# Kernel optimization log

Hardware: AMD Instinct MI355X
Metric: run time of the kernel (lower is better)

## Reference

```python
import jax, jax.numpy as jnp
import numpy as np

N_NODES = 100000


def gcn_conv(x, src, dst, W, b, n_nodes):
    """PyG GCNConv: out = D^{-1/2} (A + I) D^{-1/2} X W + b (self-loops added)."""
    h = x @ W  # [N, out]
    loops = jnp.arange(n_nodes, dtype=src.dtype)
    s = jnp.concatenate([src, loops])
    d = jnp.concatenate([dst, loops])
    deg = jax.ops.segment_sum(jnp.ones_like(d, dtype=h.dtype), d, num_segments=n_nodes)
    dinv = jnp.where(deg > 0, jax.lax.rsqrt(deg), 0.0)
    norm = dinv[s] * dinv[d]  # [E+N]
    msgs = norm[:, None] * h[s]  # gather + scale
    out = jax.ops.segment_sum(msgs, d, num_segments=n_nodes)
    return out + b


def setup_inputs() -> dict:
    key = jax.random.key(0)
    ks = jax.random.split(key, 10)
    n, e, f_in = N_NODES, 1600000, 128
    x = jax.random.normal(ks[0], (n, f_in), dtype=jnp.float32)
    edge_index = jax.random.randint(ks[1], (2, e), 0, n, dtype=jnp.int64)
    dims = [f_in, 15, 20, 27, 36]
    params = {}
    for i in range(4):
        fan_in, fan_out = dims[i], dims[i + 1]
        scale = 1.0 / np.sqrt(fan_in)
        params[f"W{i+1}"] = jax.random.uniform(ks[2 + 2 * i], (fan_in, fan_out), minval=-scale, maxval=scale, dtype=jnp.float32)
        params[f"b{i+1}"] = jax.random.uniform(ks[3 + 2 * i], (fan_out,), minval=-scale, maxval=scale, dtype=jnp.float32)
    return {"x": x, "edge_index": edge_index, **params}


def reference(x, edge_index, W1, b1, W2, b2, W3, b3, W4, b4):
    src, dst = edge_index[0], edge_index[1]
    n = x.shape[0]
    h = jax.nn.selu(gcn_conv(x, src, dst, W1, b1, n))
    h = jax.nn.selu(gcn_conv(h, src, dst, W2, b2, n))
    h = jax.nn.selu(gcn_conv(h, src, dst, W3, b3, n))
    h = jax.nn.selu(gcn_conv(h, src, dst, W4, b4, n))
    return h
```

## Files before the change

kernel.cpp:

```cpp
#include <hip/hip_runtime.h>
#include <hip/hip_fp16.h>
#include <math.h>

#define BLK 256
#define CBSH 9
#define CBN 512
#define NCBC 256
#define NB2 512

__device__ __forceinline__ float selu_f(float x) {
    const float kScale = 1.0507009873554805f;
    const float kAlpha = 1.6732632423543772f;
    return x > 0.0f ? kScale * x : kScale * kAlpha * expm1f(x);
}

__device__ __forceinline__ float2 h2f2(unsigned u) {
    __half2 h = *reinterpret_cast<__half2*>(&u);
    return __half22float2(h);
}
__device__ __forceinline__ void h8_set(float* a, uint4 v) {
    float2 f0 = h2f2(v.x), f1 = h2f2(v.y), f2 = h2f2(v.z), f3 = h2f2(v.w);
    a[0] = f0.x; a[1] = f0.y; a[2] = f1.x; a[3] = f1.y;
    a[4] = f2.x; a[5] = f2.y; a[6] = f3.x; a[7] = f3.y;
}
__device__ __forceinline__ void h8_add(float* a, uint4 v) {
    float2 f0 = h2f2(v.x), f1 = h2f2(v.y), f2 = h2f2(v.z), f3 = h2f2(v.w);
    a[0] += f0.x; a[1] += f0.y; a[2] += f1.x; a[3] += f1.y;
    a[4] += f2.x; a[5] += f2.y; a[6] += f3.x; a[7] += f3.y;
}

__global__ void k_cnt(const int* __restrict__ dst, int* __restrict__ H, int e, int nbkt) {
    __shared__ int hist[NCBC];
    int tid = threadIdx.x;
    for (int b = tid; b < nbkt; b += BLK) hist[b] = 0;
    __syncthreads();
    int per = (e + NB2 - 1) / NB2;
    int lo = blockIdx.x * per;
    int hi = min(e, lo + per);
    for (int i = lo + tid; i < hi; i += BLK) atomicAdd(&hist[dst[i] >> CBSH], 1);
    __syncthreads();
    for (int b = tid; b < nbkt; b += BLK) H[blockIdx.x * nbkt + b] = hist[b];
}

__global__ void k_bsum(const int* __restrict__ H, int* __restrict__ bstart, int nbkt, int e) {
    __shared__ int tot[NCBC];
    int tid = threadIdx.x;
    for (int b = tid; b < nbkt; b += BLK) {
        int s = 0;
        for (int i = 0; i < NB2; ++i) s += H[i * nbkt + b];
        tot[b] = s;
    }
    __syncthreads();
    if (tid == 0) {
        int acc = 0;
        for (int b = 0; b < nbkt; ++b) {
            bstart[b] = acc;
            acc += tot[b];
        }
        bstart[nbkt] = acc;
    }
}

__global__ void k_off(int* __restrict__ H, const int* __restrict__ bstart, int nbkt) {
    __shared__ int lds[BLK];
    int b = blockIdx.x, tid = threadIdx.x;
    int v0 = H[(2 * tid) * nbkt + b];
    int v1 = H[(2 * tid + 1) * nbkt + b];
    int pair = v0 + v1;
    lds[tid] = pair;
    __syncthreads();
    int val = pair;
    for (int off = 1; off < BLK; off <<= 1) {
        int t2 = (tid >= off) ? lds[tid - off] : 0;
        __syncthreads();
        val += t2;
        lds[tid] = val;
        __syncthreads();
    }
    int excl = val - pair + bstart[b];
    H[(2 * tid) * nbkt + b] = excl;
    H[(2 * tid + 1) * nbkt + b] = excl + v0;
}

__global__ void k_scatter2(const int* __restrict__ src, const int* __restrict__ dst,
                           const int* __restrict__ H, unsigned* __restrict__ slab,
                           int e, int nbkt) {
    __shared__ int cur[NCBC];
    int tid = threadIdx.x;
    for (int b = tid; b < nbkt; b += BLK) cur[b] = H[blockIdx.x * nbkt + b];
    __syncthreads();
    int per = (e + NB2 - 1) / NB2;
    int lo = blockIdx.x * per;
    int hi = min(e, lo + per);
    for (int i = lo + tid; i < hi; i += BLK) {
        int s = src[i], d = dst[i];
        int b = d >> CBSH;
        int pos = atomicAdd(&cur[b], 1);
        slab[pos] = ((unsigned)s << CBSH) | (unsigned)(d & (CBN - 1));
    }
}

__global__ void k_build(const int* __restrict__ bstart, const unsigned* __restrict__ slab,
                        int* __restrict__ rowptr, float* __restrict__ dinv,
                        int* __restrict__ csr, int n, int e) {
    __shared__ int hist[CBN];
    __shared__ int stmp[BLK];
    int b = blockIdx.x, tid = threadIdx.x;
    hist[2 * tid] = 0;
    hist[2 * tid + 1] = 0;
    __syncthreads();
    int lo = bstart[b], hi = bstart[b + 1];
    for (int i = lo + tid; i < hi; i += BLK) atomicAdd(&hist[slab[i] & (CBN - 1)], 1);
    __syncthreads();
    int h0 = hist[2 * tid], h1 = hist[2 * tid + 1];
    int pair = h0 + h1;
    stmp[tid] = pair;
    __syncthreads();
    int val = pair;
    for (int off = 1; off < BLK; off <<= 1) {
        int t2 = (tid >= off) ? stmp[tid - off] : 0;
        __syncthreads();
        val += t2;
        stmp[tid] = val;
        __syncthreads();
    }
    int e0 = lo + val - pair;
    int e1 = e0 + h0;
    hist[2 * tid] = e0;
    hist[2 * tid + 1] = e1;
    int node0 = b << CBSH;
    int nA = node0 + 2 * tid, nB = nA + 1;
    if (nA < n) { rowptr[nA] = e0; dinv[nA] = rsqrtf((float)(h0 + 1)); }
    if (nB < n) { rowptr[nB] = e1; dinv[nB] = rsqrtf((float)(h1 + 1)); }
    if (b == 0 && tid == 0) rowptr[n] = e;
    __syncthreads();
    for (int i = lo + tid; i < hi; i += BLK) {
        unsigned p = slab[i];
        int pos = atomicAdd(&hist[p & (CBN - 1)], 1);
        csr[pos] = (int)(p >> CBSH);
    }
}

template <int K, int KP, int F, int SI, int SO, bool FUSE_IN>
__global__ void k_gemm(const float* __restrict__ xin, const float* __restrict__ W,
                       const float* __restrict__ bprev, const float* __restrict__ dinv,
                       __half* __restrict__ hs, int n) {
    constexpr int F8 = (F + 7) & ~7;
    int i = blockIdx.x * BLK + threadIdx.x;
    if (i >= n) return;
    const float* xr = xin + (size_t)i * SI;
    float di = dinv[i];
    float accf[F8];
#pragma unroll
    for (int f = 0; f < F8; ++f) accf[f] = 0.0f;
#pragma unroll
    for (int k4 = 0; k4 < KP / 4; ++k4) {
        float4 xv = *reinterpret_cast<const float4*>(xr + k4 * 4);
        float xs4[4] = {xv.x, xv.y, xv.z, xv.w};
#pragma unroll
        for (int j = 0; j < 4; ++j) {
            const int k = k4 * 4 + j;
            if (k < K) {
                float xval = xs4[j];
                if (FUSE_IN) xval = selu_f(di * xval + bprev[k]);
#pragma unroll
                for (int f = 0; f < F; ++f) accf[f] = fmaf(xval, W[k * F + f], accf[f]);
            }
        }
    }
#pragma unroll
    for (int f = 0; f < F; ++f) accf[f] *= di;
    __half2* ro2 = reinterpret_cast<__half2*>(hs + (size_t)i * SO);
#pragma unroll
    for (int f2 = 0; f2 < F8 / 2; ++f2)
        ro2[f2] = __float22half2_rn(make_float2(accf[2 * f2], accf[2 * f2 + 1]));
}

__global__ void k_gemm4(const float* __restrict__ xin, const float* __restrict__ W,
                        const float* __restrict__ bprev, const float* __restrict__ dinv,
                        __half* __restrict__ hsm, __half* __restrict__ hst, int n) {
    constexpr int K = 27, F = 36;
    int i = blockIdx.x * BLK + threadIdx.x;
    if (i >= n) return;
    const float* xr = xin + (size_t)i * 32;
    float di = dinv[i];
    float accf[40];
#pragma unroll
    for (int f = 0; f < 40; ++f) accf[f] = 0.0f;
#pragma unroll
    for (int k4 = 0; k4 < 7; ++k4) {
        float4 xv = *reinterpret_cast<const float4*>(xr + k4 * 4);
        float xs4[4] = {xv.x, xv.y, xv.z, xv.w};
#pragma unroll
        for (int j = 0; j < 4; ++j) {
            const int k = k4 * 4 + j;
            if (k < K) {
                float xval = selu_f(di * xv.x + bprev[k]);
                xval = selu_f(di * xs4[j] + bprev[k]);
#pragma unroll
                for (int f = 0; f < F; ++f) accf[f] = fmaf(xval, W[k * F + f], accf[f]);
            }
        }
    }
#pragma unroll
    for (int f = 0; f < F; ++f) accf[f] *= di;
    __half2* rm = reinterpret_cast<__half2*>(hsm + (size_t)i * 32);
#pragma unroll
    for (int f2 = 0; f2 < 16; ++f2)
        rm[f2] = __float22half2_rn(make_float2(accf[2 * f2], accf[2 * f2 + 1]));
    __half2* rt = reinterpret_cast<__half2*>(hst + (size_t)i * 8);
#pragma unroll
    for (int f2 = 0; f2 < 4; ++f2)
        rt[f2] = __float22half2_rn(make_float2(accf[32 + 2 * f2], accf[32 + 2 * f2 + 1]));
}

template <int F, int S , int G, int SOUT>
__global__ void k_agg(const int* __restrict__ rowptr, const int* __restrict__ csr,
                      const __half* __restrict__ hs, float* __restrict__ out, int n) {
    constexpr int NPW = 64 / G;
    constexpr int CH = ((F + 7) & ~7) / 8;
    int lane = threadIdx.x & 63;
    int g = lane / G;
    int fl = lane & (G - 1);
    int wid = (blockIdx.x * BLK + threadIdx.x) >> 6;
    int d = wid * NPW + g;
    if (d >= n || fl >= CH) return;
    int beg = rowptr[d], end = rowptr[d + 1];
    auto rowp = [&](int r) {
        return reinterpret_cast<const uint4*>(hs + (size_t)r * S) + fl;
    };
    float s0[8], s1[8] = {0}, s2[8] = {0}, s3[8] = {0};
    h8_set(s0, *rowp(d));
    int p = beg;
    for (; p + 8 <= end; p += 8) {
        int e0 = __builtin_nontemporal_load(csr + p);
        int e1 = __builtin_nontemporal_load(csr + p + 1);
        int e2 = __builtin_nontemporal_load(csr + p + 2);
        int e3 = __builtin_nontemporal_load(csr + p + 3);
        int e4 = __builtin_nontemporal_load(csr + p + 4);
        int e5 = __builtin_nontemporal_load(csr + p + 5);
        int e6 = __builtin_nontemporal_load(csr + p + 6);
        int e7 = __builtin_nontemporal_load(csr + p + 7);
        uint4 v0 = *rowp(e0), v1 = *rowp(e1), v2 = *rowp(e2), v3 = *rowp(e3);
        uint4 v4 = *rowp(e4), v5 = *rowp(e5), v6 = *rowp(e6), v7 = *rowp(e7);
        h8_add(s0, v0); h8_add(s1, v1); h8_add(s2, v2); h8_add(s3, v3);
        h8_add(s0, v4); h8_add(s1, v5); h8_add(s2, v6); h8_add(s3, v7);
    }
    for (; p + 4 <= end; p += 4) {
        int e0 = __builtin_nontemporal_load(csr + p);
        int e1 = __builtin_nontemporal_load(csr + p + 1);
        int e2 = __builtin_nontemporal_load(csr + p + 2);
        int e3 = __builtin_nontemporal_load(csr + p + 3);
        uint4 v0 = *rowp(e0), v1 = *rowp(e1), v2 = *rowp(e2), v3 = *rowp(e3);
        h8_add(s0, v0); h8_add(s1, v1); h8_add(s2, v2); h8_add(s3, v3);
    }
    for (; p < end; ++p) h8_add(s0, *rowp(__builtin_nontemporal_load(csr + p)));
    float sum[8];
#pragma unroll
    for (int j = 0; j < 8; ++j) sum[j] = (s0[j] + s1[j]) + (s2[j] + s3[j]);
    float* op = out + (size_t)d * SOUT + fl * 8;
    *reinterpret_cast<float4*>(op) = make_float4(sum[0], sum[1], sum[2], sum[3]);
    *reinterpret_cast<float4*>(op + 4) = make_float4(sum[4], sum[5], sum[6], sum[7]);
}

__global__ void k_agg4(const int* __restrict__ rowptr, const int* __restrict__ csr,
                       const __half* __restrict__ hsm, const __half* __restrict__ hst,
                       float* __restrict__ out, const float* __restrict__ dinv,
                       const float* __restrict__ bias, int n) {
    constexpr int G = 8, NPW = 8;
    int lane = threadIdx.x & 63;
    int g = lane / G;
    int fl = lane & (G - 1);
    int wid = (blockIdx.x * BLK + threadIdx.x) >> 6;
    int d = wid * NPW + g;
    if (d >= n || fl >= 5) return;
    int beg = rowptr[d], end = rowptr[d + 1];
    const __half* bp = (fl < 4) ? hsm + fl * 8 : hst;
    int mul = (fl < 4) ? 32 : 8;
    auto rowp = [&](int r) {
        return reinterpret_cast<const uint4*>(bp + (size_t)r * mul);
    };
    float s0[8], s1[8] = {0}, s2[8] = {0}, s3[8] = {0};
    h8_set(s0, *rowp(d));
    int p = beg;
    for (; p + 8 <= end; p += 8) {
        int e0 = __builtin_nontemporal_load(csr + p);
        int e1 = __builtin_nontemporal_load(csr + p + 1);
        int e2 = __builtin_nontemporal_load(csr + p + 2);
        int e3 = __builtin_nontemporal_load(csr + p + 3);
        int e4 = __builtin_nontemporal_load(csr + p + 4);
        int e5 = __builtin_nontemporal_load(csr + p + 5);
        int e6 = __builtin_nontemporal_load(csr + p + 6);
        int e7 = __builtin_nontemporal_load(csr + p + 7);
        uint4 v0 = *rowp(e0), v1 = *rowp(e1), v2 = *rowp(e2), v3 = *rowp(e3);
        uint4 v4 = *rowp(e4), v5 = *rowp(e5), v6 = *rowp(e6), v7 = *rowp(e7);
        h8_add(s0, v0); h8_add(s1, v1); h8_add(s2, v2); h8_add(s3, v3);
        h8_add(s0, v4); h8_add(s1, v5); h8_add(s2, v6); h8_add(s3, v7);
    }
    for (; p + 4 <= end; p += 4) {
        int e0 = __builtin_nontemporal_load(csr + p);
        int e1 = __builtin_nontemporal_load(csr + p + 1);
        int e2 = __builtin_nontemporal_load(csr + p + 2);
        int e3 = __builtin_nontemporal_load(csr + p + 3);
        uint4 v0 = *rowp(e0), v1 = *rowp(e1), v2 = *rowp(e2), v3 = *rowp(e3);
        h8_add(s0, v0); h8_add(s1, v1); h8_add(s2, v2); h8_add(s3, v3);
    }
    for (; p < end; ++p) h8_add(s0, *rowp(__builtin_nontemporal_load(csr + p)));
    float dv = dinv[d];
    float r[8];
#pragma unroll
    for (int j = 0; j < 8; ++j) {
        float sum = (s0[j] + s1[j]) + (s2[j] + s3[j]);
        int col = (fl < 4) ? fl * 8 + j : 32 + j;
        r[j] = (col < 36) ? selu_f(dv * sum + bias[col]) : 0.0f;
    }
    if (fl < 4) {
        float* op = out + (size_t)d * 36 + fl * 8;
        *reinterpret_cast<float4*>(op) = make_float4(r[0], r[1], r[2], r[3]);
        *reinterpret_cast<float4*>(op + 4) = make_float4(r[4], r[5], r[6], r[7]);
    } else {
        float* op = out + (size_t)d * 36 + 32;
        *reinterpret_cast<float4*>(op) = make_float4(r[0], r[1], r[2], r[3]);
    }
}

extern "C" void kernel_launch(void* const* d_in, const int* in_sizes, int n_in,
                              void* d_out, int out_size, void* d_ws, size_t ws_size,
                              hipStream_t stream) {
    const float* x = (const float*)d_in[0];
    const int* ei = (const int*)d_in[1];
    const float* W1 = (const float*)d_in[2];
    const float* b1 = (const float*)d_in[3];
    const float* W2 = (const float*)d_in[4];
    const float* b2 = (const float*)d_in[5];
    const float* W3 = (const float*)d_in[6];
    const float* b3 = (const float*)d_in[7];
    const float* W4 = (const float*)d_in[8];
    const float* b4 = (const float*)d_in[9];

    int n = in_sizes[0] / 128;
    int e = in_sizes[1] / 2;
    const int* s32 = ei;
    const int* d32 = ei + e;
    int nbkt = (n + CBN - 1) >> CBSH;

    char* w = (char*)d_ws;
    auto alloc = [&](size_t bytes) {
        char* p = w;
        w += (bytes + 255) & ~(size_t)255;
        return p;
    };
    int* rowptr = (int*)alloc(((size_t)n + 1) * 4);
    float* dinv = (float*)alloc((size_t)n * 4);
    int* csr = (int*)alloc((size_t)e * 4);
    int* H = (int*)alloc((size_t)NB2 * nbkt * 4);
    int* bstart = (int*)alloc(((size_t)nbkt + 1) * 4);
    __half* bufA = (__half*)alloc((size_t)n * 40 * 2);
    float* bufB = (float*)alloc((size_t)n * 32 * 4);
    unsigned* slab = (unsigned*)bufA;
    __half* hsm = bufA;
    __half* hst = bufA + (size_t)n * 32;

    int nb = (n + BLK - 1) / BLK;

    k_cnt<<<NB2, BLK, 0, stream>>>(d32, H, e, nbkt);
    k_bsum<<<1, BLK, 0, stream>>>(H, bstart, nbkt, e);
    k_off<<<nbkt, BLK, 0, stream>>>(H, bstart, nbkt);
    k_scatter2<<<NB2, BLK, 0, stream>>>(s32, d32, H, slab, e, nbkt);
    k_build<<<nbkt, BLK, 0, stream>>>(bstart, slab, rowptr, dinv, csr, n, e);

    int ab1 = (n + 127) / 128;
    int ab2 = (n + 63) / 64;
    int ab4 = (n + 31) / 32;

    k_gemm<128, 128, 15, 128, 16, false><<<nb, BLK, 0, stream>>>(x, W1, nullptr, dinv, bufA, n);
    k_agg<15, 16, 2, 16><<<ab1, BLK, 0, stream>>>(rowptr, csr, bufA, bufB, n);

    k_gemm<15, 16, 20, 16, 32, true><<<nb, BLK, 0, stream>>>(bufB, W2, b1, dinv, bufA, n);
    k_agg<20, 32, 4, 32><<<ab2, BLK, 0, stream>>>(rowptr, csr, bufA, bufB, n);

    k_gemm<20, 20, 27, 32, 32, true><<<nb, BLK, 0, stream>>>(bufB, W3, b2, dinv, bufA, n);
    k_agg<27, 32, 4, 32><<<ab2, BLK, 0, stream>>>(rowptr, csr, bufA, bufB, n);

    k_gemm4<<<nb, BLK, 0, stream>>>(bufB, W4, b3, dinv, hsm, hst, n);
    k_agg4<<<ab4, BLK, 0, stream>>>(rowptr, csr, hsm, hst, (float*)d_out, dinv, b4, n);
}
```

Before: 277.4 us.

## Reorder GCN layers to aggregate before transform using chunked fp16 feature layout

Layers 2-4 now aggregate the smaller input features first and apply the weight matrix afterwards (A·X then W), since for growing widths (15→20→27→36) aggregating narrower inputs moves fewer bytes per edge. Features are stored in a chunk-major layout of 8-half uint4 slices, with one thread per node per chunk, in place of the wavefront-group gather. The normalisation, bias and SELU are fused into the transform epilogue. The cost is an extra fp32 intermediate buffer and more blocks that each re-read the CSR indices once per chunk.

```diff
diff --git a/kernel.cpp b/kernel.cpp
--- a/kernel.cpp
+++ b/kernel.cpp
@@ -27,6 +27,18 @@
     float2 f0 = h2f2(v.x), f1 = h2f2(v.y), f2 = h2f2(v.z), f3 = h2f2(v.w);
     a[0] += f0.x; a[1] += f0.y; a[2] += f1.x; a[3] += f1.y;
     a[4] += f2.x; a[5] += f2.y; a[6] += f3.x; a[7] += f3.y;
+}
+__device__ __forceinline__ uint4 f8_pack(const float* a) {
+    __half2 h0 = __float22half2_rn(make_float2(a[0], a[1]));
+    __half2 h1 = __float22half2_rn(make_float2(a[2], a[3]));
+    __half2 h2 = __float22half2_rn(make_float2(a[4], a[5]));
+    __half2 h3 = __float22half2_rn(make_float2(a[6], a[7]));
+    uint4 u;
+    u.x = *reinterpret_cast<unsigned*>(&h0);
+    u.y = *reinterpret_cast<unsigned*>(&h1);
+    u.z = *reinterpret_cast<unsigned*>(&h2);
+    u.w = *reinterpret_cast<unsigned*>(&h3);
+    return u;
 }
 
 __global__ void k_cnt(const int* __restrict__ dst, int* __restrict__ H, int e, int nbkt) {
@@ -141,187 +153,145 @@
     }
 }
 
-template <int K, int KP, int F, int SI, int SO, bool FUSE_IN>
-__global__ void k_gemm(const float* __restrict__ xin, const float* __restrict__ W,
-                       const float* __restrict__ bprev, const float* __restrict__ dinv,
-                       __half* __restrict__ hs, int n) {
-    constexpr int F8 = (F + 7) & ~7;
+
+__global__ void k_gemm1(const float* __restrict__ x, const float* __restrict__ W,
+                        const float* __restrict__ dinv, uint4* __restrict__ G, int n) {
     int i = blockIdx.x * BLK + threadIdx.x;
     if (i >= n) return;
-    const float* xr = xin + (size_t)i * SI;
+    const float* xr = x + (size_t)i * 128;
+    float acc[16];
+#pragma unroll
+    for (int f = 0; f < 16; ++f) acc[f] = 0.0f;
+#pragma unroll
+    for (int k4 = 0; k4 < 32; ++k4) {
+        float4 xv = *reinterpret_cast<const float4*>(xr + k4 * 4);
+        float xs[4] = {xv.x, xv.y, xv.z, xv.w};
+#pragma unroll
+        for (int j = 0; j < 4; ++j) {
+            int k = k4 * 4 + j;
+#pragma unroll
+            for (int f = 0; f < 15; ++f) acc[f] = fmaf(xs[j], W[k * 15 + f], acc[f]);
+        }
+    }
     float di = dinv[i];
-    float accf[F8];
-#pragma unroll
-    for (int f = 0; f < F8; ++f) accf[f] = 0.0f;
-#pragma unroll
-    for (int k4 = 0; k4 < KP / 4; ++k4) {
-        float4 xv = *reinterpret_cast<const float4*>(xr + k4 * 4);
-        float xs4[4] = {xv.x, xv.y, xv.z, xv.w};
-#pragma unroll
-        for (int j = 0; j < 4; ++j) {
-            const int k = k4 * 4 + j;
-            if (k < K) {
-                float xval = xs4[j];
-                if (FUSE_IN) xval = selu_f(di * xval + bprev[k]);
-#pragma unroll
-                for (int f = 0; f < F; ++f) accf[f] = fmaf(xval, W[k * F + f], accf[f]);
-            }
-        }
-    }
-#pragma unroll
-    for (int f = 0; f < F; ++f) accf[f] *= di;
-    __half2* ro2 = reinterpret_cast<__half2*>(hs + (size_t)i * SO);
-#pragma unroll
-    for (int f2 = 0; f2 < F8 / 2; ++f2)
-        ro2[f2] = __float22half2_rn(make_float2(accf[2 * f2], accf[2 * f2 + 1]));
-}
-
-__global__ void k_gemm4(const float* __restrict__ xin, const float* __restrict__ W,
-                        const float* __restrict__ bprev, const float* __restrict__ dinv,
-                        __half* __restrict__ hsm, __half* __restrict__ hst, int n) {
-    constexpr int K = 27, F = 36;
+#pragma unroll
+    for (int f = 0; f < 15; ++f) acc[f] *= di;
+    acc[15] = 0.0f;
+    G[i] = f8_pack(acc);
+    G[(size_t)n + i] = f8_pack(acc + 8);
+}
+
+__global__ void k_aggF(const int* __restrict__ rowptr, const int* __restrict__ csr,
+                       const uint4* __restrict__ hs, uint4* __restrict__ G2,
+                       const float* __restrict__ dinv, const float* __restrict__ bias, int n) {
+    int chunk = blockIdx.x & 1;
+    int d = (blockIdx.x >> 1) * BLK + threadIdx.x;
+    if (d >= n) return;
+    const uint4* gs = hs + (size_t)chunk * n;
+    float a0[8], a1[8] = {0};
+    h8_set(a0, gs[d]);
+    int p = rowptr[d], end = rowptr[d + 1];
+    for (; p + 4 <= end; p += 4) {
+        int r0 = csr[p], r1 = csr[p + 1], r2 = csr[p + 2], r3 = csr[p + 3];
+        uint4 v0 = gs[r0], v1 = gs[r1], v2 = gs[r2], v3 = gs[r3];
+        h8_add(a0, v0); h8_add(a1, v1); h8_add(a0, v2); h8_add(a1, v3);
+    }
+    for (; p < end; ++p) h8_add(a0, gs[csr[p]]);
+    float di = dinv[d];
+    float g[8];
+    int colb = chunk * 8;
+#pragma unroll
+    for (int j = 0; j < 8; ++j) {
+        int col = colb + j;
+        float s = a0[j] + a1[j];
+        g[j] = (col < 15) ? di * selu_f(di * s + bias[col]) : 0.0f;
+    }
+    G2[(size_t)chunk * n + d] = f8_pack(g);
+}
+
+template <int CHM, int FCH>
+__global__ void k_aggK(const int* __restrict__ rowptr, const int* __restrict__ csr,
+                       const uint4* __restrict__ G, float4* __restrict__ A, int n) {
+    int chunk = blockIdx.x & (CHM - 1);
+    int d = (blockIdx.x / CHM) * BLK + threadIdx.x;
+    if (d >= n) return;
+    if (FCH < CHM && chunk >= FCH) return;
+    const uint4* gs = G + (size_t)chunk * n;
+    float a0[8], a1[8] = {0};
+    h8_set(a0, gs[d]);
+    int p = rowptr[d], end = rowptr[d + 1];
+    for (; p + 4 <= end; p += 4) {
+        int r0 = csr[p], r1 = csr[p + 1], r2 = csr[p + 2], r3 = csr[p + 3];
+        uint4 v0 = gs[r0], v1 = gs[r1], v2 = gs[r2], v3 = gs[r3];
+        h8_add(a0, v0); h8_add(a1, v1); h8_add(a0, v2); h8_add(a1, v3);
+    }
+    for (; p < end; ++p) h8_add(a0, gs[csr[p]]);
+    size_t o = ((size_t)chunk * n + d) * 2;
+    A[o] = make_float4(a0[0] + a1[0], a0[1] + a1[1], a0[2] + a1[2], a0[3] + a1[3]);
+    A[o + 1] = make_float4(a0[4] + a1[4], a0[5] + a1[5], a0[6] + a1[6], a0[7] + a1[7]);
+}
+
+template <int KCH, int K, int F, int FCH>
+__global__ void k_gemmM(const float* __restrict__ A, const float* __restrict__ W,
+                        const float* __restrict__ bias, const float* __restrict__ dinv,
+                        uint4* __restrict__ G, int n) {
     int i = blockIdx.x * BLK + threadIdx.x;
     if (i >= n) return;
-    const float* xr = xin + (size_t)i * 32;
+    const float4* A4 = reinterpret_cast<const float4*>(A);
+    float xr[KCH * 8];
+#pragma unroll
+    for (int c = 0; c < KCH; ++c) {
+        size_t o = ((size_t)c * n + i) * 2;
+        float4 lo = A4[o], hi = A4[o + 1];
+        xr[c * 8 + 0] = lo.x; xr[c * 8 + 1] = lo.y; xr[c * 8 + 2] = lo.z; xr[c * 8 + 3] = lo.w;
+        xr[c * 8 + 4] = hi.x; xr[c * 8 + 5] = hi.y; xr[c * 8 + 6] = hi.z; xr[c * 8 + 7] = hi.w;
+    }
+    float acc[F];
+#pragma unroll
+    for (int f = 0; f < F; ++f) acc[f] = 0.0f;
+#pragma unroll
+    for (int k = 0; k < K; ++k)
+#pragma unroll
+        for (int f = 0; f < F; ++f) acc[f] = fmaf(xr[k], W[k * F + f], acc[f]);
     float di = dinv[i];
-    float accf[40];
-#pragma unroll
-    for (int f = 0; f < 40; ++f) accf[f] = 0.0f;
-#pragma unroll
-    for (int k4 = 0; k4 < 7; ++k4) {
-        float4 xv = *reinterpret_cast<const float4*>(xr + k4 * 4);
-        float xs4[4] = {xv.x, xv.y, xv.z, xv.w};
-#pragma unroll
-        for (int j = 0; j < 4; ++j) {
-            const int k = k4 * 4 + j;
-            if (k < K) {
-                float xval = selu_f(di * xv.x + bprev[k]);
-                xval = selu_f(di * xs4[j] + bprev[k]);
-#pragma unroll
-                for (int f = 0; f < F; ++f) accf[f] = fmaf(xval, W[k * F + f], accf[f]);
-            }
-        }
-    }
-#pragma unroll
-    for (int f = 0; f < F; ++f) accf[f] *= di;
-    __half2* rm = reinterpret_cast<__half2*>(hsm + (size_t)i * 32);
-#pragma unroll
-    for (int f2 = 0; f2 < 16; ++f2)
-        rm[f2] = __float22half2_rn(make_float2(accf[2 * f2], accf[2 * f2 + 1]));
-    __half2* rt = reinterpret_cast<__half2*>(hst + (size_t)i * 8);
-#pragma unroll
-    for (int f2 = 0; f2 < 4; ++f2)
-        rt[f2] = __float22half2_rn(make_float2(accf[32 + 2 * f2], accf[32 + 2 * f2 + 1]));
-}
-
-template <int F, int S , int G, int SOUT>
-__global__ void k_agg(const int* __restrict__ rowptr, const int* __restrict__ csr,
-                      const __half* __restrict__ hs, float* __restrict__ out, int n) {
-    constexpr int NPW = 64 / G;
-    constexpr int CH = ((F + 7) & ~7) / 8;
-    int lane = threadIdx.x & 63;
-    int g = lane / G;
-    int fl = lane & (G - 1);
-    int wid = (blockIdx.x * BLK + threadIdx.x) >> 6;
-    int d = wid * NPW + g;
-    if (d >= n || fl >= CH) return;
-    int beg = rowptr[d], end = rowptr[d + 1];
-    auto rowp = [&](int r) {
-        return reinterpret_cast<const uint4*>(hs + (size_t)r * S) + fl;
-    };
-    float s0[8], s1[8] = {0}, s2[8] = {0}, s3[8] = {0};
-    h8_set(s0, *rowp(d));
-    int p = beg;
-    for (; p + 8 <= end; p += 8) {
-        int e0 = __builtin_nontemporal_load(csr + p);
-        int e1 = __builtin_nontemporal_load(csr + p + 1);
-        int e2 = __builtin_nontemporal_load(csr + p + 2);
-        int e3 = __builtin_nontemporal_load(csr + p + 3);
-        int e4 = __builtin_nontemporal_load(csr + p + 4);
-        int e5 = __builtin_nontemporal_load(csr + p + 5);
-        int e6 = __builtin_nontemporal_load(csr + p + 6);
-        int e7 = __builtin_nontemporal_load(csr + p + 7);
-        uint4 v0 = *rowp(e0), v1 = *rowp(e1), v2 = *rowp(e2), v3 = *rowp(e3);
-        uint4 v4 = *rowp(e4), v5 = *rowp(e5), v6 = *rowp(e6), v7 = *rowp(e7);
-        h8_add(s0, v0); h8_add(s1, v1); h8_add(s2, v2); h8_add(s3, v3);
-        h8_add(s0, v4); h8_add(s1, v5); h8_add(s2, v6); h8_add(s3, v7);
-    }
-    for (; p + 4 <= end; p += 4) {
-        int e0 = __builtin_nontemporal_load(csr + p);
-        int e1 = __builtin_nontemporal_load(csr + p + 1);
-        int e2 = __builtin_nontemporal_load(csr + p + 2);
-        int e3 = __builtin_nontemporal_load(csr + p + 3);
-        uint4 v0 = *rowp(e0), v1 = *rowp(e1), v2 = *rowp(e2), v3 = *rowp(e3);
-        h8_add(s0, v0); h8_add(s1, v1); h8_add(s2, v2); h8_add(s3, v3);
-    }
-    for (; p < end; ++p) h8_add(s0, *rowp(__builtin_nontemporal_load(csr + p)));
-    float sum[8];
-#pragma unroll
-    for (int j = 0; j < 8; ++j) sum[j] = (s0[j] + s1[j]) + (s2[j] + s3[j]);
-    float* op = out + (size_t)d * SOUT + fl * 8;
-    *reinterpret_cast<float4*>(op) = make_float4(sum[0], sum[1], sum[2], sum[3]);
-    *reinterpret_cast<float4*>(op + 4) = make_float4(sum[4], sum[5], sum[6], sum[7]);
-}
-
-__global__ void k_agg4(const int* __restrict__ rowptr, const int* __restrict__ csr,
-                       const __half* __restrict__ hsm, const __half* __restrict__ hst,
-                       float* __restrict__ out, const float* __restrict__ dinv,
-                       const float* __restrict__ bias, int n) {
-    constexpr int G = 8, NPW = 8;
-    int lane = threadIdx.x & 63;
-    int g = lane / G;
-    int fl = lane & (G - 1);
-    int wid = (blockIdx.x * BLK + threadIdx.x) >> 6;
-    int d = wid * NPW + g;
-    if (d >= n || fl >= 5) return;
-    int beg = rowptr[d], end = rowptr[d + 1];
-    const __half* bp = (fl < 4) ? hsm + fl * 8 : hst;
-    int mul = (fl < 4) ? 32 : 8;
-    auto rowp = [&](int r) {
-        return reinterpret_cast<const uint4*>(bp + (size_t)r * mul);
-    };
-    float s0[8], s1[8] = {0}, s2[8] = {0}, s3[8] = {0};
-    h8_set(s0, *rowp(d));
-    int p = beg;
-    for (; p + 8 <= end; p += 8) {
-        int e0 = __builtin_nontemporal_load(csr + p);
-        int e1 = __builtin_nontemporal_load(csr + p + 1);
-        int e2 = __builtin_nontemporal_load(csr + p + 2);
-        int e3 = __builtin_nontemporal_load(csr + p + 3);
-        int e4 = __builtin_nontemporal_load(csr + p + 4);
-        int e5 = __builtin_nontemporal_load(csr + p + 5);
-        int e6 = __builtin_nontemporal_load(csr + p + 6);
-        int e7 = __builtin_nontemporal_load(csr + p + 7);
-        uint4 v0 = *rowp(e0), v1 = *rowp(e1), v2 = *rowp(e2), v3 = *rowp(e3);
-        uint4 v4 = *rowp(e4), v5 = *rowp(e5), v6 = *rowp(e6), v7 = *rowp(e7);
-        h8_add(s0, v0); h8_add(s1, v1); h8_add(s2, v2); h8_add(s3, v3);
-        h8_add(s0, v4); h8_add(s1, v5); h8_add(s2, v6); h8_add(s3, v7);
-    }
-    for (; p + 4 <= end; p += 4) {
-        int e0 = __builtin_nontemporal_load(csr + p);
-        int e1 = __builtin_nontemporal_load(csr + p + 1);
-        int e2 = __builtin_nontemporal_load(csr + p + 2);
-        int e3 = __builtin_nontemporal_load(csr + p + 3);
-        uint4 v0 = *rowp(e0), v1 = *rowp(e1), v2 = *rowp(e2), v3 = *rowp(e3);
-        h8_add(s0, v0); h8_add(s1, v1); h8_add(s2, v2); h8_add(s3, v3);
-    }
-    for (; p < end; ++p) h8_add(s0, *rowp(__builtin_nontemporal_load(csr + p)));
-    float dv = dinv[d];
-    float r[8];
-#pragma unroll
-    for (int j = 0; j < 8; ++j) {
-        float sum = (s0[j] + s1[j]) + (s2[j] + s3[j]);
-        int col = (fl < 4) ? fl * 8 + j : 32 + j;
-        r[j] = (col < 36) ? selu_f(dv * sum + bias[col]) : 0.0f;
-    }
-    if (fl < 4) {
-        float* op = out + (size_t)d * 36 + fl * 8;
-        *reinterpret_cast<float4*>(op) = make_float4(r[0], r[1], r[2], r[3]);
-        *reinterpret_cast<float4*>(op + 4) = make_float4(r[4], r[5], r[6], r[7]);
-    } else {
-        float* op = out + (size_t)d * 36 + 32;
-        *reinterpret_cast<float4*>(op) = make_float4(r[0], r[1], r[2], r[3]);
-    }
+    float g[FCH * 8];
+#pragma unroll
+    for (int idx = 0; idx < FCH * 8; ++idx)
+        g[idx] = (idx < F) ? di * selu_f(di * acc[idx] + bias[idx]) : 0.0f;
+#pragma unroll
+    for (int c = 0; c < FCH; ++c) G[(size_t)c * n + i] = f8_pack(g + c * 8);
+}
+
+__global__ void k_gemm4(const float* __restrict__ A, const float* __restrict__ W,
+                        const float* __restrict__ bias, const float* __restrict__ dinv,
+                        float* __restrict__ out, int n) {
+    int i = blockIdx.x * BLK + threadIdx.x;
+    if (i >= n) return;
+    const float4* A4 = reinterpret_cast<const float4*>(A);
+    float xr[32];
+#pragma unroll
+    for (int c = 0; c < 4; ++c) {
+        size_t o = ((size_t)c * n + i) * 2;
+        float4 lo = A4[o], hi = A4[o + 1];
+        xr[c * 8 + 0] = lo.x; xr[c * 8 + 1] = lo.y; xr[c * 8 + 2] = lo.z; xr[c * 8 + 3] = lo.w;
+        xr[c * 8 + 4] = hi.x; xr[c * 8 + 5] = hi.y; xr[c * 8 + 6] = hi.z; xr[c * 8 + 7] = hi.w;
+    }
+    float acc[36];
+#pragma unroll
+    for (int f = 0; f < 36; ++f) acc[f] = 0.0f;
+#pragma unroll
+    for (int k = 0; k < 27; ++k)
+#pragma unroll
+        for (int f = 0; f < 36; ++f) acc[f] = fmaf(xr[k], W[k * 36 + f], acc[f]);
+    float di = dinv[i];
+    float r[36];
+#pragma unroll
+    for (int f = 0; f < 36; ++f) r[f] = selu_f(di * acc[f] + bias[f]);
+    float* op = out + (size_t)i * 36;
+#pragma unroll
+    for (int f4 = 0; f4 < 9; ++f4)
+        *reinterpret_cast<float4*>(op + f4 * 4) =
+            make_float4(r[f4 * 4], r[f4 * 4 + 1], r[f4 * 4 + 2], r[f4 * 4 + 3]);
 }
 
 extern "C" void kernel_launch(void* const* d_in, const int* in_sizes, int n_in,
@@ -355,13 +325,13 @@
     int* csr = (int*)alloc((size_t)e * 4);
     int* H = (int*)alloc((size_t)NB2 * nbkt * 4);
     int* bstart = (int*)alloc(((size_t)nbkt + 1) * 4);
-    __half* bufA = (__half*)alloc((size_t)n * 40 * 2);
-    float* bufB = (float*)alloc((size_t)n * 32 * 4);
-    unsigned* slab = (unsigned*)bufA;
-    __half* hsm = bufA;
-    __half* hst = bufA + (size_t)n * 32;
+    uint4* Gu1 = (uint4*)alloc((size_t)n * 4 * 16);
+    uint4* Gu2 = (uint4*)alloc((size_t)n * 4 * 16);
+    float* A = (float*)alloc((size_t)n * 4 * 8 * 4);
+    unsigned* slab = (unsigned*)Gu1;
 
     int nb = (n + BLK - 1) / BLK;
+    int nbn = nb;
 
     k_cnt<<<NB2, BLK, 0, stream>>>(d32, H, e, nbkt);
     k_bsum<<<1, BLK, 0, stream>>>(H, bstart, nbkt, e);
@@ -369,19 +339,15 @@
     k_scatter2<<<NB2, BLK, 0, stream>>>(s32, d32, H, slab, e, nbkt);
     k_build<<<nbkt, BLK, 0, stream>>>(bstart, slab, rowptr, dinv, csr, n, e);
 
-    int ab1 = (n + 127) / 128;
-    int ab2 = (n + 63) / 64;
-    int ab4 = (n + 31) / 32;
-
-    k_gemm<128, 128, 15, 128, 16, false><<<nb, BLK, 0, stream>>>(x, W1, nullptr, dinv, bufA, n);
-    k_agg<15, 16, 2, 16><<<ab1, BLK, 0, stream>>>(rowptr, csr, bufA, bufB, n);
-
-    k_gemm<15, 16, 20, 16, 32, true><<<nb, BLK, 0, stream>>>(bufB, W2, b1, dinv, bufA, n);
-    k_agg<20, 32, 4, 32><<<ab2, BLK, 0, stream>>>(rowptr, csr, bufA, bufB, n);
-
-    k_gemm<20, 20, 27, 32, 32, true><<<nb, BLK, 0, stream>>>(bufB, W3, b2, dinv, bufA, n);
-    k_agg<27, 32, 4, 32><<<ab2, BLK, 0, stream>>>(rowptr, csr, bufA, bufB, n);
-
-    k_gemm4<<<nb, BLK, 0, stream>>>(bufB, W4, b3, dinv, hsm, hst, n);
-    k_agg4<<<ab4, BLK, 0, stream>>>(rowptr, csr, hsm, hst, (float*)d_out, dinv, b4, n);
-}
+    k_gemm1<<<nb, BLK, 0, stream>>>(x, W1, dinv, Gu2, n);
+    k_aggF<<<2 * nbn, BLK, 0, stream>>>(rowptr, csr, Gu2, Gu1, dinv, b1, n);
+
+    k_aggK<2, 2><<<2 * nbn, BLK, 0, stream>>>(rowptr, csr, Gu1, (float4*)A, n);
+    k_gemmM<2, 15, 20, 3><<<nb, BLK, 0, stream>>>(A, W2, b2, dinv, Gu2, n);
+
+    k_aggK<4, 3><<<4 * nbn, BLK, 0, stream>>>(rowptr, csr, Gu2, (float4*)A, n);
+    k_gemmM<3, 20, 27, 4><<<nb, BLK, 0, stream>>>(A, W3, b3, dinv, Gu1, n);
+
+    k_aggK<4, 4><<<4 * nbn, BLK, 0, stream>>>(rowptr, csr, Gu1, (float4*)A, n);
+    k_gemm4<<<nb, BLK, 0, stream>>>(A, W4, b4, dinv, (float*)d_out, n);
+}
```

Result: slower. 345.4 us (+24.5%).

## Split layer-4 features into five column slabs, aggregate one slab per thread

Applied to the files above, without the earlier changes.

The last layer's transformed features are now stored as five separate column-major slabs of 8 halves each, replacing the interleaved 32+8 layout. The final aggregation runs one thread per (node, slab) with a blockIdx class index, so each slab's random gathers hit a smaller working set that may fit better in cache. A redundant selu computation in the layer-4 GEMM is also removed. The trade-off is five passes over the CSR indices instead of one, three of every eight blocks launched only to exit, and per-thread serial neighbour loops.

```diff
diff --git a/kernel.cpp b/kernel.cpp
--- a/kernel.cpp
+++ b/kernel.cpp
@@ -27,6 +27,18 @@
     float2 f0 = h2f2(v.x), f1 = h2f2(v.y), f2 = h2f2(v.z), f3 = h2f2(v.w);
     a[0] += f0.x; a[1] += f0.y; a[2] += f1.x; a[3] += f1.y;
     a[4] += f2.x; a[5] += f2.y; a[6] += f3.x; a[7] += f3.y;
+}
+__device__ __forceinline__ uint4 f8_pack(const float* a) {
+    __half2 h0 = __float22half2_rn(make_float2(a[0], a[1]));
+    __half2 h1 = __float22half2_rn(make_float2(a[2], a[3]));
+    __half2 h2 = __float22half2_rn(make_float2(a[4], a[5]));
+    __half2 h3 = __float22half2_rn(make_float2(a[6], a[7]));
+    uint4 u;
+    u.x = *reinterpret_cast<unsigned*>(&h0);
+    u.y = *reinterpret_cast<unsigned*>(&h1);
+    u.z = *reinterpret_cast<unsigned*>(&h2);
+    u.w = *reinterpret_cast<unsigned*>(&h3);
+    return u;
 }
 
 __global__ void k_cnt(const int* __restrict__ dst, int* __restrict__ H, int e, int nbkt) {
@@ -178,7 +190,7 @@
 
 __global__ void k_gemm4(const float* __restrict__ xin, const float* __restrict__ W,
                         const float* __restrict__ bprev, const float* __restrict__ dinv,
-                        __half* __restrict__ hsm, __half* __restrict__ hst, int n) {
+                        uint4* __restrict__ G, int n) {
     constexpr int K = 27, F = 36;
     int i = blockIdx.x * BLK + threadIdx.x;
     if (i >= n) return;
@@ -195,8 +207,7 @@
         for (int j = 0; j < 4; ++j) {
             const int k = k4 * 4 + j;
             if (k < K) {
-                float xval = selu_f(di * xv.x + bprev[k]);
-                xval = selu_f(di * xs4[j] + bprev[k]);
+                float xval = selu_f(di * xs4[j] + bprev[k]);
 #pragma unroll
                 for (int f = 0; f < F; ++f) accf[f] = fmaf(xval, W[k * F + f], accf[f]);
             }
@@ -204,14 +215,10 @@
     }
 #pragma unroll
     for (int f = 0; f < F; ++f) accf[f] *= di;
-    __half2* rm = reinterpret_cast<__half2*>(hsm + (size_t)i * 32);
-#pragma unroll
-    for (int f2 = 0; f2 < 16; ++f2)
-        rm[f2] = __float22half2_rn(make_float2(accf[2 * f2], accf[2 * f2 + 1]));
-    __half2* rt = reinterpret_cast<__half2*>(hst + (size_t)i * 8);
-#pragma unroll
-    for (int f2 = 0; f2 < 4; ++f2)
-        rt[f2] = __float22half2_rn(make_float2(accf[32 + 2 * f2], accf[32 + 2 * f2 + 1]));
+#pragma unroll
+    for (int f = F; f < 40; ++f) accf[f] = 0.0f;
+#pragma unroll
+    for (int c = 0; c < 5; ++c) G[(size_t)c * n + i] = f8_pack(accf + c * 8);
 }
 
 template <int F, int S , int G, int SOUT>
@@ -263,64 +270,47 @@
     *reinterpret_cast<float4*>(op + 4) = make_float4(sum[4], sum[5], sum[6], sum[7]);
 }
 
-__global__ void k_agg4(const int* __restrict__ rowptr, const int* __restrict__ csr,
-                       const __half* __restrict__ hsm, const __half* __restrict__ hst,
-                       float* __restrict__ out, const float* __restrict__ dinv,
-                       const float* __restrict__ bias, int n) {
-    constexpr int G = 8, NPW = 8;
-    int lane = threadIdx.x & 63;
-    int g = lane / G;
-    int fl = lane & (G - 1);
-    int wid = (blockIdx.x * BLK + threadIdx.x) >> 6;
-    int d = wid * NPW + g;
-    if (d >= n || fl >= 5) return;
-    int beg = rowptr[d], end = rowptr[d + 1];
-    const __half* bp = (fl < 4) ? hsm + fl * 8 : hst;
-    int mul = (fl < 4) ? 32 : 8;
-    auto rowp = [&](int r) {
-        return reinterpret_cast<const uint4*>(bp + (size_t)r * mul);
-    };
-    float s0[8], s1[8] = {0}, s2[8] = {0}, s3[8] = {0};
-    h8_set(s0, *rowp(d));
-    int p = beg;
-    for (; p + 8 <= end; p += 8) {
-        int e0 = __builtin_nontemporal_load(csr + p);
-        int e1 = __builtin_nontemporal_load(csr + p + 1);
-        int e2 = __builtin_nontemporal_load(csr + p + 2);
-        int e3 = __builtin_nontemporal_load(csr + p + 3);
-        int e4 = __builtin_nontemporal_load(csr + p + 4);
-        int e5 = __builtin_nontemporal_load(csr + p + 5);
-        int e6 = __builtin_nontemporal_load(csr + p + 6);
-        int e7 = __builtin_nontemporal_load(csr + p + 7);
-        uint4 v0 = *rowp(e0), v1 = *rowp(e1), v2 = *rowp(e2), v3 = *rowp(e3);
-        uint4 v4 = *rowp(e4), v5 = *rowp(e5), v6 = *rowp(e6), v7 = *rowp(e7);
-        h8_add(s0, v0); h8_add(s1, v1); h8_add(s2, v2); h8_add(s3, v3);
-        h8_add(s0, v4); h8_add(s1, v5); h8_add(s2, v6); h8_add(s3, v7);
-    }
+__global__ void k_agg4s(const int* __restrict__ rowptr, const int* __restrict__ csr,
+                        const uint4* __restrict__ G, float* __restrict__ out,
+                        const float* __restrict__ dinv, const float* __restrict__ bias,
+                        int n) {
+    int cls = blockIdx.x & 7;
+    if (cls >= 5) return;
+    int d = (blockIdx.x >> 3) * BLK + threadIdx.x;
+    if (d >= n) return;
+    const uint4* gs = G + (size_t)cls * n;
+    float a0[8], a1[8] = {0}, a2[8] = {0}, a3[8] = {0};
+    h8_set(a0, gs[d]);
+    int p = rowptr[d], end = rowptr[d + 1];
     for (; p + 4 <= end; p += 4) {
-        int e0 = __builtin_nontemporal_load(csr + p);
-        int e1 = __builtin_nontemporal_load(csr + p + 1);
-        int e2 = __builtin_nontemporal_load(csr + p + 2);
-        int e3 = __builtin_nontemporal_load(csr + p + 3);
-        uint4 v0 = *rowp(e0), v1 = *rowp(e1), v2 = *rowp(e2), v3 = *rowp(e3);
-        h8_add(s0, v0); h8_add(s1, v1); h8_add(s2, v2); h8_add(s3, v3);
-    }
-    for (; p < end; ++p) h8_add(s0, *rowp(__builtin_nontemporal_load(csr + p)));
-    float dv = dinv[d];
-    float r[8];
-#pragma unroll
-    for (int j = 0; j < 8; ++j) {
-        float sum = (s0[j] + s1[j]) + (s2[j] + s3[j]);
-        int col = (fl < 4) ? fl * 8 + j : 32 + j;
-        r[j] = (col < 36) ? selu_f(dv * sum + bias[col]) : 0.0f;
-    }
-    if (fl < 4) {
-        float* op = out + (size_t)d * 36 + fl * 8;
+        int r0 = __builtin_nontemporal_load(csr + p);
+        int r1 = __builtin_nontemporal_load(csr + p + 1);
+        int r2 = __builtin_nontemporal_load(csr + p + 2);
+        int r3 = __builtin_nontemporal_load(csr + p + 3);
+        uint4 v0 = gs[r0], v1 = gs[r1], v2 = gs[r2], v3 = gs[r3];
+        h8_add(a0, v0); h8_add(a1, v1); h8_add(a2, v2); h8_add(a3, v3);
+    }
+    for (; p < end; ++p) h8_add(a0, gs[__builtin_nontemporal_load(csr + p)]);
+    float di = dinv[d];
+    if (cls < 4) {
+        float r[8];
+#pragma unroll
+        for (int j = 0; j < 8; ++j) {
+            float s = (a0[j] + a1[j]) + (a2[j] + a3[j]);
+            r[j] = selu_f(di * s + bias[cls * 8 + j]);
+        }
+        float* op = out + (size_t)d * 36 + cls * 8;
         *reinterpret_cast<float4*>(op) = make_float4(r[0], r[1], r[2], r[3]);
         *reinterpret_cast<float4*>(op + 4) = make_float4(r[4], r[5], r[6], r[7]);
     } else {
-        float* op = out + (size_t)d * 36 + 32;
-        *reinterpret_cast<float4*>(op) = make_float4(r[0], r[1], r[2], r[3]);
+        float r[4];
+#pragma unroll
+        for (int j = 0; j < 4; ++j) {
+            float s = (a0[j] + a1[j]) + (a2[j] + a3[j]);
+            r[j] = selu_f(di * s + bias[32 + j]);
+        }
+        *reinterpret_cast<float4*>(out + (size_t)d * 36 + 32) =
+            make_float4(r[0], r[1], r[2], r[3]);
     }
 }
 
@@ -358,8 +348,7 @@
     __half* bufA = (__half*)alloc((size_t)n * 40 * 2);
     float* bufB = (float*)alloc((size_t)n * 32 * 4);
     unsigned* slab = (unsigned*)bufA;
-    __half* hsm = bufA;
-    __half* hst = bufA + (size_t)n * 32;
+    uint4* G4 = (uint4*)bufA;
 
     int nb = (n + BLK - 1) / BLK;
 
@@ -371,7 +360,6 @@
 
     int ab1 = (n + 127) / 128;
     int ab2 = (n + 63) / 64;
-    int ab4 = (n + 31) / 32;
 
     k_gemm<128, 128, 15, 128, 16, false><<<nb, BLK, 0, stream>>>(x, W1, nullptr, dinv, bufA, n);
     k_agg<15, 16, 2, 16><<<ab1, BLK, 0, stream>>>(rowptr, csr, bufA, bufB, n);
@@ -382,6 +370,6 @@
     k_gemm<20, 20, 27, 32, 32, true><<<nb, BLK, 0, stream>>>(bufB, W3, b2, dinv, bufA, n);
     k_agg<27, 32, 4, 32><<<ab2, BLK, 0, stream>>>(rowptr, csr, bufA, bufB, n);
 
-    k_gemm4<<<nb, BLK, 0, stream>>>(bufB, W4, b3, dinv, hsm, hst, n);
-    k_agg4<<<ab4, BLK, 0, stream>>>(rowptr, csr, hsm, hst, (float*)d_out, dinv, b4, n);
-}
+    k_gemm4<<<nb, BLK, 0, stream>>>(bufB, W4, b3, dinv, G4, n);
+    k_agg4s<<<8 * nb, BLK, 0, stream>>>(rowptr, csr, G4, (float*)d_out, dinv, b4, n);
+}
```

Measured after the change: 345.5 us. +24.6%, slower.
